# Optimization experiments

Measured on AMD Instinct MI355X. Metric: run time of the kernel, lower is better.

Reference implementation:

```python
import jax, jax.numpy as jnp
import numpy as np

V = 32000   # vocab
E = 512     # hidden_size (d_model)
NH = 8      # num_heads
DH = E // NH
NL = 2      # num_layers
FF = 2048   # TransformerDecoderLayer default dim_feedforward
MAXLEN = 24 # cfg.max_length -> gen_len (no target given)
S, B = 48, 8
TRANS = 14
INIT = TRANS - 2            # tgt = transform[1:-1]
LF = INIT + MAXLEN - 1      # final tgt length after the loop
EPS = 1e-5
NEG = -1e9


def pos_encoding(length, d):
    pos = np.arange(length, dtype=np.float32)[:, None]
    div = np.exp(-np.log(10000.0) * np.arange(0, d, 2, dtype=np.float32) / d)
    pe = np.zeros((length, d), dtype=np.float32)
    pe[:, 0::2] = np.sin(pos * div)
    pe[:, 1::2] = np.cos(pos * div)
    return jnp.asarray(pe)


def setup_inputs() -> dict:
    key = jax.random.key(0)
    ks = jax.random.split(key, 12)
    s = 0.02
    return {
        "enc_outputs": jax.random.normal(ks[0], (S, B, E), jnp.float32),
        "transform": jax.random.randint(ks[1], (TRANS, B), 0, V),
        "tf_ratio": 0,
        "emb_table": jax.random.normal(ks[2], (V, E), jnp.float32) * s,
        "sa_w": jax.random.normal(ks[3], (NL, 3 * E, E), jnp.float32) * s,
        "sa_b": jnp.zeros((NL, 3 * E), jnp.float32),
        "sa_ow": jax.random.normal(ks[4], (NL, E, E), jnp.float32) * s,
        "sa_ob": jnp.zeros((NL, E), jnp.float32),
        "ca_w": jax.random.normal(ks[5], (NL, 3 * E, E), jnp.float32) * s,
        "ca_b": jnp.zeros((NL, 3 * E), jnp.float32),
        "ca_ow": jax.random.normal(ks[6], (NL, E, E), jnp.float32) * s,
        "ca_ob": jnp.zeros((NL, E), jnp.float32),
        "ff1_w": jax.random.normal(ks[7], (NL, FF, E), jnp.float32) * s,
        "ff1_b": jnp.zeros((NL, FF), jnp.float32),
        "ff2_w": jax.random.normal(ks[8], (NL, E, FF), jnp.float32) * s,
        "ff2_b": jnp.zeros((NL, E), jnp.float32),
        "ln_g": jnp.ones((NL, 3, E), jnp.float32),
        "ln_b": jnp.zeros((NL, 3, E), jnp.float32),
        "out_w": jax.random.normal(ks[9], (V, E), jnp.float32) * s,
        "out_b": jnp.zeros((V,), jnp.float32),
    }


def _ln(x, g, b):
    m = jnp.mean(x, -1, keepdims=True)
    v = jnp.mean((x - m) ** 2, -1, keepdims=True)
    return (x - m) * jax.lax.rsqrt(v + EPS) * g + b


def _mha(q_in, kv_in, w, b, ow, ob, mask):
    # q_in [Lq,B,E], kv_in [Lk,B,E]; PyTorch packed in_proj [3E,E]
    wq, wk, wv = jnp.split(w, 3, 0)
    bq, bk, bv = jnp.split(b, 3, 0)
    proj = lambda x, wm, bm: (x @ wm.T + bm).reshape(x.shape[0], x.shape[1], NH, DH)
    q, k, v = proj(q_in, wq, bq), proj(kv_in, wk, bk), proj(kv_in, wv, bv)
    sc = jnp.einsum('qbhd,kbhd->bhqk', q, k) / np.sqrt(DH).astype(np.float32)
    if mask is not None:
        sc = sc + mask
    a = jax.nn.softmax(sc, -1)
    o = jnp.einsum('bhqk,kbhd->qbhd', a, v).reshape(q_in.shape[0], q_in.shape[1], E)
    return o @ ow.T + ob


def _decoder(x, mem, mask, p):
    # post-norm TransformerDecoderLayer: self-attn -> cross-attn -> relu FFN
    for l in range(NL):
        x = _ln(x + _mha(x, x, p['sa_w'][l], p['sa_b'][l], p['sa_ow'][l], p['sa_ob'][l], mask),
                p['ln_g'][l, 0], p['ln_b'][l, 0])
        x = _ln(x + _mha(x, mem, p['ca_w'][l], p['ca_b'][l], p['ca_ow'][l], p['ca_ob'][l], None),
                p['ln_g'][l, 1], p['ln_b'][l, 1])
        h = jax.nn.relu(x @ p['ff1_w'][l].T + p['ff1_b'][l]) @ p['ff2_w'][l].T + p['ff2_b'][l]
        x = _ln(x + h, p['ln_g'][l, 2], p['ln_b'][l, 2])
    return x


def reference(enc_outputs, transform, tf_ratio, emb_table, sa_w, sa_b, sa_ow, sa_ob,
              ca_w, ca_b, ca_ow, ca_ob, ff1_w, ff1_b, ff2_w, ff2_b, ln_g, ln_b,
              out_w, out_b):
    # tf_ratio == 0 -> no teacher forcing; gen_len = max_length (no target attr)
    p = dict(sa_w=sa_w, sa_b=sa_b, sa_ow=sa_ow, sa_ob=sa_ob, ca_w=ca_w, ca_b=ca_b,
             ca_ow=ca_ow, ca_ob=ca_ob, ff1_w=ff1_w, ff1_b=ff1_b, ff2_w=ff2_w,
             ff2_b=ff2_b, ln_g=ln_g, ln_b=ln_b)
    pe = pos_encoding(MAXLEN, E)
    # causal mask over the fixed-size buffer; padded (future) slots cannot
    # influence valid positions, so full-buffer passes == torch prefix passes.
    mask = jnp.where(jnp.tril(jnp.ones((LF, LF), bool)), 0.0, NEG)
    tgt0 = emb_table[transform[1:-1]] + pe[:INIT][:, None, :]   # [INIT,B,E]
    buf = jnp.zeros((LF, B, E), jnp.float32).at[:INIT].set(tgt0)

    def step(buf, i):
        h = _decoder(buf, enc_outputs, mask, p)
        pos = INIT - 1 + i                        # last valid position
        pred = jnp.argmax(h[pos] @ out_w.T + out_b, axis=-1)   # [B]
        # torch re-embeds the single predicted token -> PE position 0
        emb = emb_table[pred] + pe[0]
        return buf.at[pos + 1].set(emb), None

    buf, _ = jax.lax.scan(step, buf, jnp.arange(MAXLEN - 1))
    h = _decoder(buf, enc_outputs, mask, p)       # final loop iteration's pass
    return h @ out_w.T + out_b                    # dec_outputs [LF,B,V]
```

## Files before the change

### kernel.cpp

```cpp
#include <hip/hip_runtime.h>
#include <hip/hip_bf16.h>
#include <math.h>

#define V    32000
#define E    512
#define NH   8
#define DH   64
#define NL   2
#define FF   2048
#define MAXLEN 24
#define S    48
#define B    8
#define TRANS 14
#define INIT 12
#define LF   35

#define NB   256
#define NT   1024

typedef float f4 __attribute__((ext_vector_type(4)));

__device__ inline float wsum(float v) {
#pragma unroll
  for (int off = 32; off; off >>= 1) v += __shfl_xor(v, off);
  return v;
}
__device__ inline float wmax(float v) {
#pragma unroll
  for (int off = 32; off; off >>= 1) v = fmaxf(v, __shfl_xor(v, off));
  return v;
}

__device__ inline void stc(float* p, float v) {
  __hip_atomic_store(p, v, __ATOMIC_RELAXED, __HIP_MEMORY_SCOPE_AGENT);
}
__device__ inline void stc8(float* p, float x, float y) {
  union { unsigned long long u; float f[2]; } c; c.f[0] = x; c.f[1] = y;
  __hip_atomic_store((unsigned long long*)p, c.u, __ATOMIC_RELAXED, __HIP_MEMORY_SCOPE_AGENT);
}
__device__ inline int ldci(const int* p) {
  return __hip_atomic_load(p, __ATOMIC_RELAXED, __HIP_MEMORY_SCOPE_AGENT);
}
__device__ inline void stci(int* p, int v) {
  __hip_atomic_store(p, v, __ATOMIC_RELAXED, __HIP_MEMORY_SCOPE_AGENT);
}

#define CMB(v, idx, ov, oi) do { if ((ov) > (v) || ((ov) == (v) && (oi) < (idx))) { (v) = (ov); (idx) = (oi); } } while (0)


__global__ void embed_init_k(const int* __restrict__ transform, const float* __restrict__ emb,
                             float* __restrict__ xbuf) {
  int t = blockIdx.x;
  int pos = t >> 3, b = t & 7;
  int tok = transform[(1 + pos) * B + b];
  for (int d = threadIdx.x; d < E; d += blockDim.x) {
    double div = exp(-log(10000.0) * (double)(d & ~1) / (double)E);
    double ang = (double)pos * div;
    float pe = (d & 1) ? (float)cos(ang) : (float)sin(ang);
    xbuf[(size_t)t * E + d] = emb[(size_t)tok * E + d] + pe;
  }
}

template <int K>
__global__ __launch_bounds__(256) void gemm_k(
    const float* __restrict__ x, const float* __restrict__ W, const float* __restrict__ bias,
    int ntok, int nout, int route, int relu,
    float* __restrict__ out0, float* __restrict__ out1, float* __restrict__ out2) {
  constexpr int K4 = K / 4;
  constexpr int J  = K / 256;
  __shared__ float4 xt[8][K4];
  const int tid = threadIdx.x;
  const int lane = tid & 63;
  const int o = blockIdx.x * 4 + (tid >> 6);

  float4 wr[J];
  if (o < nout) {
    const float4* Wr = (const float4*)(W + (size_t)o * K);
#pragma unroll
    for (int j = 0; j < J; ++j) wr[j] = Wr[lane + 64 * j];
  }

  const int ng = ntok >> 3;
  for (int g = 0; g < ng; ++g) {
    if (g) __syncthreads();
    const float4* xg = (const float4*)(x + (size_t)g * 8 * K);
    float4* xf = &xt[0][0];
    for (int i = tid; i < 8 * K4; i += 256) xf[i] = xg[i];
    __syncthreads();
    if (o < nout) {
      float acc[8] = {0, 0, 0, 0, 0, 0, 0, 0};
#pragma unroll
      for (int j = 0; j < J; ++j) {
        float4 w = wr[j];
#pragma unroll
        for (int tt = 0; tt < 8; ++tt) {
          float4 xv = xt[tt][lane + 64 * j];
          acc[tt] += w.x * xv.x + w.y * xv.y + w.z * xv.z + w.w * xv.w;
        }
      }
#pragma unroll
      for (int tt = 0; tt < 8; ++tt) acc[tt] = wsum(acc[tt]);
      if (lane == 0) {
        float bo = bias[o];
#pragma unroll
        for (int tt = 0; tt < 8; ++tt) {
          float v = acc[tt] + bo;
          if (relu) v = fmaxf(v, 0.f);
          int t = g * 8 + tt;
          if (route == 0) {
            out0[(size_t)t * nout + o] = v;
          } else if (route == 1) {
            if (o < E) out0[(size_t)t * E + o] = v;
            else if (o < 2 * E) out1[(size_t)t * E + (o - E)] = v;
            else out2[(size_t)t * E + (o - 2 * E)] = v;
          } else {
            if (o < E) out0[(size_t)t * E + o] = v;
            else out1[(size_t)t * E + (o - E)] = v;
          }
        }
      }
    }
  }
}

__global__ __launch_bounds__(256) void attn_k(
    const float* __restrict__ q, const float* __restrict__ Kc, const float* __restrict__ Vc,
    float* __restrict__ outp, int p0, int nq, int nk_fixed, int causal) {
  const int tid = threadIdx.x;
  const int lane = tid & 63;
  const int u = blockIdx.x * 4 + (tid >> 6);
  if (u >= nq * 64) return;
  const int qi = u >> 6;
  const int r = u & 63;
  const int b = r >> 3, h = r & 7;
  const int nk = causal ? (p0 + qi + 1) : nk_fixed;

  const size_t qoff = (size_t)(qi * B + b) * E + h * DH + lane;
  const float qv = q[qoff];

  float myscore = -INFINITY;
  for (int k = 0; k < nk; ++k) {
    float prod = qv * Kc[(size_t)(k * B + b) * E + h * DH + lane];
    prod = wsum(prod);
    if (lane == k) myscore = prod * 0.125f;
  }
  float m = wmax(myscore);
  float p = (lane < nk) ? expf(myscore - m) : 0.f;
  float denom = wsum(p);
  float a = p / denom;

  float oacc = 0.f;
  for (int k = 0; k < nk; ++k) {
    float ak = __shfl(a, k);
    oacc = fmaf(ak, Vc[(size_t)(k * B + b) * E + h * DH + lane], oacc);
  }
  outp[qoff] = oacc;
}

__global__ __launch_bounds__(256) void add_ln_k(
    const float* __restrict__ xa, const float* __restrict__ xb,
    const float* __restrict__ g, const float* __restrict__ beta,
    float* __restrict__ outp, int ntok) {
  const int tid = threadIdx.x, lane = tid & 63;
  const int t = blockIdx.x * 4 + (tid >> 6);
  if (t >= ntok) return;
  float v[8];
  float s = 0.f;
#pragma unroll
  for (int j = 0; j < 8; ++j) {
    int d = lane + 64 * j;
    v[j] = xa[(size_t)t * E + d] + xb[(size_t)t * E + d];
    s += v[j];
  }
  s = wsum(s);
  float mean = s * (1.f / 512.f);
  float d2 = 0.f;
#pragma unroll
  for (int j = 0; j < 8; ++j) { float dd = v[j] - mean; d2 += dd * dd; }
  d2 = wsum(d2);
  float inv = 1.f / sqrtf(d2 * (1.f / 512.f) + 1e-5f);
#pragma unroll
  for (int j = 0; j < 8; ++j) {
    int d = lane + 64 * j;
    outp[(size_t)t * E + d] = (v[j] - mean) * inv * g[d] + beta[d];
  }
}

#define B_QKV 0
#define B_OW  6144
#define B_CQ  8192
#define B_COW 10240
#define B_FF1 12288
#define B_FF2 20480
#define SW_TOT 28672
#define SLOTS_PER_STEP 23
#define NSTAGE 17

__global__ __launch_bounds__(NT, 1) void decode_persist_k(
    const float* __restrict__ emb,
    const float* __restrict__ sa_w, const float* __restrict__ sa_b,
    const float* __restrict__ sa_ow, const float* __restrict__ sa_ob,
    const float* __restrict__ ca_w, const float* __restrict__ ca_b,
    const float* __restrict__ ca_ow, const float* __restrict__ ca_ob,
    const float* __restrict__ ff1_w, const float* __restrict__ ff1_b,
    const float* __restrict__ ff2_w, const float* __restrict__ ff2_b,
    const float* __restrict__ ln_g, const float* __restrict__ ln_b,
    const float* __restrict__ out_w, const float* __restrict__ out_b,
    float* __restrict__ kself, float* __restrict__ vself,
    const float* __restrict__ kcross, const float* __restrict__ vcross,
    float* __restrict__ arena, float* __restrict__ outp, int* __restrict__ bar) {
  __shared__ __align__(16) float s_w[SW_TOT];
  __shared__ __align__(16) float s_x[8 * E];
  __shared__ __align__(16) float s_raw[8 * E];
  __shared__ __align__(16) float s_q2[64];
  __shared__ __align__(16) float s_attw[64];
  __shared__ __align__(16) float s_part[4][64];
  __shared__ int   s_tok[8];
  __shared__ float s_pv[16][8];
  __shared__ int   s_pi[16][8];

  const int tid  = threadIdx.x;
  const int lane = tid & 63;
  const int wv   = tid >> 6;
  const int bid  = blockIdx.x;

  auto slot = [&](int st, int s) -> float* {
    return arena + ((size_t)st * SLOTS_PER_STEP + s) * 4096;
  };

  auto flg = [&](int s, int j) -> int* { return &bar[(s * 256 + j) * 16]; };

  auto set_flag = [&](int s, int tgt, bool producer) {
    __syncthreads();
    if (producer && tid == 0) stci(flg(s, bid), tgt);
  };
  auto wait_flags = [&](int s, int base, int count, int tgt) {
    if (wv == 0) {
      const int m = count - 1;
      for (;;) {
        bool ok = true;
        for (int f = lane; f < count; f += 64)
          ok &= (ldci(flg(s, base + ((f + bid) & m))) >= tgt);
        if (__all(ok)) break;
        __builtin_amdgcn_s_sleep(12);
      }
    }
    __syncthreads();
  };

  auto stage_raw = [&](const float* src) {
    const float4* s4 = (const float4*)src;
    float4* d4 = (float4*)s_raw;
    for (int k = tid; k < 1024; k += NT) d4[k] = s4[k];
    __syncthreads();
  };
  auto lnstage = [&](int lnidx) {
    if (wv < 8) {
      const float* gg = ln_g + (size_t)lnidx * E;
      const float* be = ln_b + (size_t)lnidx * E;
      float v[8]; float sum = 0.f;
#pragma unroll
      for (int j = 0; j < 8; ++j) {
        int d = lane + 64 * j;
        v[j] = s_x[wv * E + d] + s_raw[wv * E + d];
        sum += v[j];
      }
      sum = wsum(sum);
      float mean = sum * (1.f / 512.f);
      float d2 = 0.f;
#pragma unroll
      for (int j = 0; j < 8; ++j) { float dd = v[j] - mean; d2 += dd * dd; }
      d2 = wsum(d2);
      float inv = 1.f / sqrtf(d2 * (1.f / 512.f) + 1e-5f);
#pragma unroll
      for (int j = 0; j < 8; ++j) {
        int d = lane + 64 * j;
        s_x[wv * E + d] = (v[j] - mean) * inv * gg[d] + be[d];
      }
    }
    __syncthreads();
  };
  auto proj16 = [&](int wbase, const float* srcLDS, const float* biasp, float* dst) {
    int j = wv & 1, b = wv >> 1;
    int r = bid * 2 + j;
    const f4* wp = (const f4*)&s_w[wbase + j * 512];
    f4 w0 = wp[lane], w1 = wp[lane + 64];
    const f4* x4 = (const f4*)(srcLDS + b * E);
    f4 a = w0 * x4[lane] + w1 * x4[lane + 64];
    float acc = a.x + a.y + a.z + a.w;
    acc = wsum(acc);
    if (lane == 0) stc(&dst[b * E + r], acc + biasp[r]);
  };
  auto attn_stage = [&](const float* qsrc, const float* Kbase, const float* Vbase,
                        int nk, float* attdst) {
    const int b = bid >> 3, h = bid & 7;
    if (wv == 0) {
      s_q2[lane] = qsrc[b * E + h * DH + lane];
      float sc = -INFINITY;
      if (lane < nk) {
        const f4* Kr = (const f4*)(Kbase + ((size_t)lane * B + b) * E + h * DH);
        const f4* Qp = (const f4*)s_q2;
        float a0 = 0.f;
#pragma unroll
        for (int u = 0; u < 16; ++u) {
          f4 kv = Kr[u], qq = Qp[u];
          a0 += kv.x * qq.x + kv.y * qq.y + kv.z * qq.z + kv.w * qq.w;
        }
        sc = a0 * 0.125f;
      }
      float m = wmax(sc);
      float e = (lane < nk) ? expf(sc - m) : 0.f;
      float den = wsum(e);
      s_attw[lane] = e / den;
    }
    __syncthreads();
    if (wv < 4) {
      float o = 0.f;
      for (int k = wv; k < nk; k += 4)
        o = fmaf(s_attw[k], Vbase[((size_t)k * B + b) * E + h * DH + lane], o);
      s_part[wv][lane] = o;
    }
    __syncthreads();
    if (wv == 0)
      stc(&attdst[b * E + h * DH + lane],
          s_part[0][lane] + s_part[1][lane] + s_part[2][lane] + s_part[3][lane]);
  };

  {
    auto cprow = [&](const float* src, int dstf) {
      f4* d = (f4*)&s_w[dstf]; const f4* s = (const f4*)src;
      for (int k = tid; k < 128; k += NT) d[k] = s[k];
    };
    for (int l = 0; l < NL; ++l) {
      for (int j = 0; j < 6; ++j)
        cprow(sa_w + ((size_t)l * 1536 + bid * 6 + j) * E, B_QKV + (l * 6 + j) * 512);
      for (int j = 0; j < 2; ++j) {
        cprow(sa_ow + ((size_t)l * 512 + bid * 2 + j) * E, B_OW + (l * 2 + j) * 512);
        cprow(ca_w + ((size_t)l * 1536 + bid * 2 + j) * E, B_CQ + (l * 2 + j) * 512);
        cprow(ca_ow + ((size_t)l * 512 + bid * 2 + j) * E, B_COW + (l * 2 + j) * 512);
      }
      for (int j = 0; j < 8; ++j)
        cprow(ff1_w + ((size_t)l * FF + bid * 8 + j) * E, B_FF1 + (l * 8 + j) * 512);
    }
    const int lf2 = bid >> 7;
    for (int j = 0; j < 4; ++j) {
      f4* d = (f4*)&s_w[B_FF2 + j * 2048];
      const f4* s = (const f4*)(ff2_w + ((size_t)lf2 * 512 + (bid & 127) * 4 + j) * FF);
      for (int k = tid; k < 512; k += NT) d[k] = s[k];
    }
    __syncthreads();
  }

  for (int i = 0; i < MAXLEN - 1; ++i) {
    const int p = INIT + i;
    const int tgt = i + 1;
    float* amax_o = slot(i, 0);

    if (i > 0) wait_flags(16, 0, 256, i);
    {
      int bw = wv & 7;
      float v = -INFINITY; int ix = 0x7fffffff;
      if (i == 0) {
        const float2* row = (const float2*)(outp + ((size_t)(INIT - 1) * B + bw) * V);
        for (int jj = lane; jj < V / 2; jj += 64) {
          float2 t = row[jj];
          CMB(v, ix, t.x, 2 * jj);
          CMB(v, ix, t.y, 2 * jj + 1);
        }
      } else {
        const float2* ap = (const float2*)slot(i - 1, 0);
#pragma unroll
        for (int t = 0; t < 4; ++t) {
          int e = lane * 4 + t;
          float2 pr = ap[e * 8 + bw];
          CMB(v, ix, pr.x, (int)pr.y);
        }
      }
#pragma unroll
      for (int off = 1; off < 64; off <<= 1) {
        float ov = __shfl_xor(v, off); int oi = __shfl_xor(ix, off);
        CMB(v, ix, ov, oi);
      }
      if (lane == 0 && wv < 8) s_tok[bw] = ix;
      __syncthreads();
      int b = tid >> 7, d0 = (tid & 127) * 4;
      int tok = s_tok[b];
      float4 ev = *(const float4*)(emb + (size_t)tok * E + d0);
      s_x[b * E + d0]     = ev.x;
      s_x[b * E + d0 + 1] = ev.y + 1.0f;
      s_x[b * E + d0 + 2] = ev.z;
      s_x[b * E + d0 + 3] = ev.w + 1.0f;
      __syncthreads();
    }

    for (int l = 0; l < NL; ++l) {
      const int sb = l * 8;
      float* Lb    = slot(i, 1 + l * 11);
      float* q_s   = Lb;
      float* att_s = Lb + 4096;
      float* raw_s = Lb + 8192;
      float* q_c   = Lb + 12288;
      float* att_c = Lb + 16384;
      float* raw_c = Lb + 20480;
      float* hb    = Lb + 24576;
      float* yb    = Lb + 40960;

      if (wv < 12) {
        int j = wv >> 1, bg = (wv & 1) * 4;
        int r = bid * 6 + j, sec = r >> 9, off = r & 511;
        const f4* wp = (const f4*)&s_w[B_QKV + (l * 6 + j) * 512];
        f4 w0 = wp[lane], w1 = wp[lane + 64];
        float bias = sa_b[(size_t)l * 1536 + r];
        for (int b = bg; b < bg + 4; ++b) {
          const f4* x4 = (const f4*)&s_x[b * E];
          f4 a = w0 * x4[lane] + w1 * x4[lane + 64];
          float acc = a.x + a.y + a.z + a.w;
          acc = wsum(acc);
          if (lane == 0) {
            acc += bias;
            if (sec == 0) stc(&q_s[b * E + off], acc);
            else if (sec == 1) stc(&kself[((size_t)(l * LF + p) * B + b) * E + off], acc);
            else stc(&vself[((size_t)(l * LF + p) * B + b) * E + off], acc);
          }
        }
      }
      set_flag(sb + 0, tgt, true);
      wait_flags(sb + 0, 0, 256, tgt);
      if (bid < 64)
        attn_stage(q_s, kself + (size_t)l * LF * B * E, vself + (size_t)l * LF * B * E,
                   p + 1, att_s);
      set_flag(sb + 1, tgt, bid < 64);
      wait_flags(sb + 1, 0, 64, tgt);
      stage_raw(att_s);
      proj16(B_OW + l * 1024, s_raw, sa_ob + (size_t)l * E, raw_s);
      set_flag(sb + 2, tgt, true);
      wait_flags(sb + 2, 0, 256, tgt);
      stage_raw(raw_s);
      lnstage(l * 3 + 0);
      proj16(B_CQ + l * 1024, s_x, ca_b + (size_t)l * 3 * E, q_c);
      set_flag(sb + 3, tgt, true);
      wait_flags(sb + 3, 0, 256, tgt);
      if (bid < 64)
        attn_stage(q_c, kcross + (size_t)l * S * B * E, vcross + (size_t)l * S * B * E,
                   S, att_c);
      set_flag(sb + 4, tgt, bid < 64);
      wait_flags(sb + 4, 0, 64, tgt);
      stage_raw(att_c);
      proj16(B_COW + l * 1024, s_raw, ca_ob + (size_t)l * E, raw_c);
      set_flag(sb + 5, tgt, true);
      wait_flags(sb + 5, 0, 256, tgt);
      stage_raw(raw_c);
      lnstage(l * 3 + 1);
      {
        int j = wv >> 1, bg = (wv & 1) * 4;
        int r = bid * 8 + j;
        const f4* wp = (const f4*)&s_w[B_FF1 + (l * 8 + j) * 512];
        f4 w0 = wp[lane], w1 = wp[lane + 64];
        float bias = ff1_b[(size_t)l * FF + r];
        for (int b = bg; b < bg + 4; ++b) {
          const f4* x4 = (const f4*)&s_x[b * E];
          f4 a = w0 * x4[lane] + w1 * x4[lane + 64];
          float acc = a.x + a.y + a.z + a.w;
          acc = wsum(acc);
          if (lane == 0) stc(&hb[b * FF + r], fmaxf(acc + bias, 0.f));
        }
      }
      set_flag(sb + 6, tgt, true);
      wait_flags(sb + 6, 0, 256, tgt);
      if ((bid >> 7) == l) {
        int b = wv >> 1, j0 = (wv & 1) * 2;
        int r0 = (bid & 127) * 4;
        const f4* h4 = (const f4*)(hb + b * FF);
        f4 hv[8];
#pragma unroll
        for (int j = 0; j < 8; ++j) hv[j] = h4[j * 64 + lane];
#pragma unroll
        for (int jr = 0; jr < 2; ++jr) {
          int rl = j0 + jr;
          const f4* wp = (const f4*)&s_w[B_FF2 + rl * 2048];
          float acc = 0.f;
#pragma unroll
          for (int j = 0; j < 8; ++j) {
            f4 w = wp[j * 64 + lane];
            acc += w.x * hv[j].x + w.y * hv[j].y + w.z * hv[j].z + w.w * hv[j].w;
          }
          acc = wsum(acc);
          if (lane == 0)
            stc(&yb[b * E + r0 + rl], acc + ff2_b[(size_t)l * 512 + r0 + rl]);
        }
      }
      set_flag(sb + 7, tgt, (bid >> 7) == l);
      wait_flags(sb + 7, l * 128, 128, tgt);
      stage_raw(yb);
      lnstage(l * 3 + 2);
    }

    {
      const int grp = lane >> 3, sub = lane & 7;
      const int idx = wv * 8 + grp;
      const bool valid = idx < 125;
      const int r = bid * 125 + idx;
      float acc[8] = {0, 0, 0, 0, 0, 0, 0, 0};
      if (valid) {
        const f4* wrow = (const f4*)(out_w + (size_t)r * E);
#pragma unroll
        for (int half = 0; half < 2; ++half) {
          f4 w8[8];
#pragma unroll
          for (int j = 0; j < 8; ++j) w8[j] = wrow[(half * 8 + j) * 8 + sub];
#pragma unroll
          for (int b = 0; b < 8; ++b) {
            const f4* x4 = (const f4*)&s_x[b * E];
            float a = 0.f;
#pragma unroll
            for (int j = 0; j < 8; ++j) {
              f4 xx = x4[(half * 8 + j) * 8 + sub];
              a += w8[j].x * xx.x + w8[j].y * xx.y + w8[j].z * xx.z + w8[j].w * xx.w;
            }
            acc[b] += a;
          }
        }
#pragma unroll
        for (int b = 0; b < 8; ++b) {
          acc[b] += __shfl_xor(acc[b], 1);
          acc[b] += __shfl_xor(acc[b], 2);
          acc[b] += __shfl_xor(acc[b], 4);
        }
        if (sub == 0) {
          float bo = out_b[r];
#pragma unroll
          for (int b = 0; b < 8; ++b) {
            acc[b] += bo;
            outp[((size_t)p * B + b) * V + r] = acc[b];
          }
        }
      }
#pragma unroll
      for (int b = 0; b < 8; ++b) {
        float v = (valid && sub == 0) ? acc[b] : -INFINITY;
        int ix = (valid && sub == 0) ? r : 0x7fffffff;
#pragma unroll
        for (int off = 1; off < 64; off <<= 1) {
          float ov = __shfl_xor(v, off); int oi = __shfl_xor(ix, off);
          CMB(v, ix, ov, oi);
        }
        if (lane == 0) { s_pv[wv][b] = v; s_pi[wv][b] = ix; }
      }
      __syncthreads();
      if (wv == 0) {
        int b = lane & 7, w2 = lane >> 3;
        float v = s_pv[w2][b]; int ix = s_pi[w2][b];
        float v2 = s_pv[w2 + 8][b]; int ix2 = s_pi[w2 + 8][b];
        CMB(v, ix, v2, ix2);
#pragma unroll
        for (int off = 8; off < 64; off <<= 1) {
          float ov = __shfl_xor(v, off); int oi = __shfl_xor(ix, off);
          CMB(v, ix, ov, oi);
        }
        if (lane < 8) stc8(&amax_o[(size_t)(bid * 8 + lane) * 2], v, (float)ix);
      }
    }
    set_flag(16, tgt, true);
  }
}

extern "C" void kernel_launch(void* const* d_in, const int* in_sizes, int n_in,
                              void* d_out, int out_size, void* d_ws, size_t ws_size,
                              hipStream_t stream) {
  const float* enc       = (const float*)d_in[0];
  const int*   transform = (const int*)d_in[1];
  const float* emb       = (const float*)d_in[3];
  const float* sa_w  = (const float*)d_in[4];
  const float* sa_b  = (const float*)d_in[5];
  const float* sa_ow = (const float*)d_in[6];
  const float* sa_ob = (const float*)d_in[7];
  const float* ca_w  = (const float*)d_in[8];
  const float* ca_b  = (const float*)d_in[9];
  const float* ca_ow = (const float*)d_in[10];
  const float* ca_ob = (const float*)d_in[11];
  const float* ff1_w = (const float*)d_in[12];
  const float* ff1_b = (const float*)d_in[13];
  const float* ff2_w = (const float*)d_in[14];
  const float* ff2_b = (const float*)d_in[15];
  const float* ln_g  = (const float*)d_in[16];
  const float* ln_b  = (const float*)d_in[17];
  const float* out_w = (const float*)d_in[18];
  const float* out_b = (const float*)d_in[19];
  float* out = (float*)d_out;

  const size_t SELF_SZ  = (size_t)LF * B * E;
  const size_t CROSS_SZ = (size_t)S * B * E;
  const size_t ARENA_SZ = (size_t)(MAXLEN - 1) * SLOTS_PER_STEP * 4096;
  const size_t FLAG_SZ  = (size_t)NSTAGE * 256 * 16;
  float* ws     = (float*)d_ws;
  float* xbuf   = ws;
  float* kself  = xbuf + (size_t)INIT * B * E;
  float* vself  = kself + NL * SELF_SZ;
  float* kcross = vself + NL * SELF_SZ;
  float* vcross = kcross + NL * CROSS_SZ;
  float* arena  = vcross + NL * CROSS_SZ;
  int*   bar    = (int*)(arena + ARENA_SZ);
  float* act1   = (float*)(bar + FLAG_SZ);
  float* act2   = act1 + 96 * E;
  float* act3   = act2 + 96 * E;
  float* ffb    = act3 + 96 * E;

  hipMemsetAsync(bar, 0, FLAG_SZ * 4, stream);

  embed_init_k<<<INIT * B, 128, 0, stream>>>(transform, emb, xbuf);

  for (int l = 0; l < NL; ++l) {
    gemm_k<E><<<(2 * E) / 4, 256, 0, stream>>>(
        enc, ca_w + ((size_t)l * 3 * E + E) * E, ca_b + (size_t)l * 3 * E + E,
        S * B, 2 * E, 2, 0, kcross + l * CROSS_SZ, vcross + l * CROSS_SZ, nullptr);
  }

  {
    const int p0 = 0, nq = INIT, ntok = nq * B;
    const float* xin = xbuf;
    for (int l = 0; l < NL; ++l) {
      const float* x = (l == 0) ? xin : act1;
      gemm_k<E><<<(3 * E) / 4, 256, 0, stream>>>(
          x, sa_w + (size_t)l * 3 * E * E, sa_b + (size_t)l * 3 * E, ntok, 3 * E, 1, 0,
          act2, kself + l * SELF_SZ, vself + l * SELF_SZ);
      attn_k<<<nq * 16, 256, 0, stream>>>(act2, kself + l * SELF_SZ, vself + l * SELF_SZ,
                                          act3, p0, nq, 0, 1);
      gemm_k<E><<<E / 4, 256, 0, stream>>>(
          act3, sa_ow + (size_t)l * E * E, sa_ob + (size_t)l * E, ntok, E, 0, 0, act2, nullptr, nullptr);
      add_ln_k<<<(ntok + 3) / 4, 256, 0, stream>>>(
          x, act2, ln_g + (size_t)l * 3 * E, ln_b + (size_t)l * 3 * E, act1, ntok);
      gemm_k<E><<<E / 4, 256, 0, stream>>>(
          act1, ca_w + (size_t)l * 3 * E * E, ca_b + (size_t)l * 3 * E, ntok, E, 0, 0, act2, nullptr, nullptr);
      attn_k<<<nq * 16, 256, 0, stream>>>(act2, kcross + l * CROSS_SZ, vcross + l * CROSS_SZ,
                                          act3, p0, nq, S, 0);
      gemm_k<E><<<E / 4, 256, 0, stream>>>(
          act3, ca_ow + (size_t)l * E * E, ca_ob + (size_t)l * E, ntok, E, 0, 0, act2, nullptr, nullptr);
      add_ln_k<<<(ntok + 3) / 4, 256, 0, stream>>>(
          act1, act2, ln_g + (size_t)l * 3 * E + E, ln_b + (size_t)l * 3 * E + E, act1, ntok);
      gemm_k<E><<<FF / 4, 256, 0, stream>>>(
          act1, ff1_w + (size_t)l * FF * E, ff1_b + (size_t)l * FF, ntok, FF, 0, 1, ffb, nullptr, nullptr);
      gemm_k<FF><<<E / 4, 256, 0, stream>>>(
          ffb, ff2_w + (size_t)l * E * FF, ff2_b + (size_t)l * E, ntok, E, 0, 0, act2, nullptr, nullptr);
      add_ln_k<<<(ntok + 3) / 4, 256, 0, stream>>>(
          act1, act2, ln_g + (size_t)l * 3 * E + 2 * E, ln_b + (size_t)l * 3 * E + 2 * E, act1, ntok);
    }
    gemm_k<E><<<V / 4, 256, 0, stream>>>(
        act1, out_w, out_b, ntok, V, 0, 0, out, nullptr, nullptr);
  }

  decode_persist_k<<<NB, NT, 0, stream>>>(
      emb, sa_w, sa_b, sa_ow, sa_ob, ca_w, ca_b, ca_ow, ca_ob,
      ff1_w, ff1_b, ff2_w, ff2_b, ln_g, ln_b, out_w, out_b,
      kself, vself, kcross, vcross, arena, out, bar);
}
```

Before: 5.071 ms.

## Fold prefill and cross-KV projection into the persistent decode kernel

Removes the separate prefill launches (cross K/V GEMMs, per-layer QKV, attention, projections, layernorms, FFN, vocab GEMM) and performs them inside the persistent kernel as extra flag-synchronised stages. The prefill argmax is also fused so the first decode step reads precomputed per-block maxima instead of rescanning the logits row. This targets the launch overhead and the serial gaps of about two dozen small kernels. In exchange the prefill runs under grid-wide flag barriers with per-block GEMV tiling, which may use the hardware less efficiently than the old dedicated GEMM kernels and adds more barrier stages.

```diff
diff --git a/kernel.cpp b/kernel.cpp
--- a/kernel.cpp
+++ b/kernel.cpp
@@ -47,7 +47,6 @@
 
 #define CMB(v, idx, ov, oi) do { if ((ov) > (v) || ((ov) == (v) && (oi) < (idx))) { (v) = (ov); (idx) = (oi); } } while (0)
 
-
 __global__ void embed_init_k(const int* __restrict__ transform, const float* __restrict__ emb,
                              float* __restrict__ xbuf) {
   int t = blockIdx.x;
@@ -61,131 +60,6 @@
   }
 }
 
-template <int K>
-__global__ __launch_bounds__(256) void gemm_k(
-    const float* __restrict__ x, const float* __restrict__ W, const float* __restrict__ bias,
-    int ntok, int nout, int route, int relu,
-    float* __restrict__ out0, float* __restrict__ out1, float* __restrict__ out2) {
-  constexpr int K4 = K / 4;
-  constexpr int J  = K / 256;
-  __shared__ float4 xt[8][K4];
-  const int tid = threadIdx.x;
-  const int lane = tid & 63;
-  const int o = blockIdx.x * 4 + (tid >> 6);
-
-  float4 wr[J];
-  if (o < nout) {
-    const float4* Wr = (const float4*)(W + (size_t)o * K);
-#pragma unroll
-    for (int j = 0; j < J; ++j) wr[j] = Wr[lane + 64 * j];
-  }
-
-  const int ng = ntok >> 3;
-  for (int g = 0; g < ng; ++g) {
-    if (g) __syncthreads();
-    const float4* xg = (const float4*)(x + (size_t)g * 8 * K);
-    float4* xf = &xt[0][0];
-    for (int i = tid; i < 8 * K4; i += 256) xf[i] = xg[i];
-    __syncthreads();
-    if (o < nout) {
-      float acc[8] = {0, 0, 0, 0, 0, 0, 0, 0};
-#pragma unroll
-      for (int j = 0; j < J; ++j) {
-        float4 w = wr[j];
-#pragma unroll
-        for (int tt = 0; tt < 8; ++tt) {
-          float4 xv = xt[tt][lane + 64 * j];
-          acc[tt] += w.x * xv.x + w.y * xv.y + w.z * xv.z + w.w * xv.w;
-        }
-      }
-#pragma unroll
-      for (int tt = 0; tt < 8; ++tt) acc[tt] = wsum(acc[tt]);
-      if (lane == 0) {
-        float bo = bias[o];
-#pragma unroll
-        for (int tt = 0; tt < 8; ++tt) {
-          float v = acc[tt] + bo;
-          if (relu) v = fmaxf(v, 0.f);
-          int t = g * 8 + tt;
-          if (route == 0) {
-            out0[(size_t)t * nout + o] = v;
-          } else if (route == 1) {
-            if (o < E) out0[(size_t)t * E + o] = v;
-            else if (o < 2 * E) out1[(size_t)t * E + (o - E)] = v;
-            else out2[(size_t)t * E + (o - 2 * E)] = v;
-          } else {
-            if (o < E) out0[(size_t)t * E + o] = v;
-            else out1[(size_t)t * E + (o - E)] = v;
-          }
-        }
-      }
-    }
-  }
-}
-
-__global__ __launch_bounds__(256) void attn_k(
-    const float* __restrict__ q, const float* __restrict__ Kc, const float* __restrict__ Vc,
-    float* __restrict__ outp, int p0, int nq, int nk_fixed, int causal) {
-  const int tid = threadIdx.x;
-  const int lane = tid & 63;
-  const int u = blockIdx.x * 4 + (tid >> 6);
-  if (u >= nq * 64) return;
-  const int qi = u >> 6;
-  const int r = u & 63;
-  const int b = r >> 3, h = r & 7;
-  const int nk = causal ? (p0 + qi + 1) : nk_fixed;
-
-  const size_t qoff = (size_t)(qi * B + b) * E + h * DH + lane;
-  const float qv = q[qoff];
-
-  float myscore = -INFINITY;
-  for (int k = 0; k < nk; ++k) {
-    float prod = qv * Kc[(size_t)(k * B + b) * E + h * DH + lane];
-    prod = wsum(prod);
-    if (lane == k) myscore = prod * 0.125f;
-  }
-  float m = wmax(myscore);
-  float p = (lane < nk) ? expf(myscore - m) : 0.f;
-  float denom = wsum(p);
-  float a = p / denom;
-
-  float oacc = 0.f;
-  for (int k = 0; k < nk; ++k) {
-    float ak = __shfl(a, k);
-    oacc = fmaf(ak, Vc[(size_t)(k * B + b) * E + h * DH + lane], oacc);
-  }
-  outp[qoff] = oacc;
-}
-
-__global__ __launch_bounds__(256) void add_ln_k(
-    const float* __restrict__ xa, const float* __restrict__ xb,
-    const float* __restrict__ g, const float* __restrict__ beta,
-    float* __restrict__ outp, int ntok) {
-  const int tid = threadIdx.x, lane = tid & 63;
-  const int t = blockIdx.x * 4 + (tid >> 6);
-  if (t >= ntok) return;
-  float v[8];
-  float s = 0.f;
-#pragma unroll
-  for (int j = 0; j < 8; ++j) {
-    int d = lane + 64 * j;
-    v[j] = xa[(size_t)t * E + d] + xb[(size_t)t * E + d];
-    s += v[j];
-  }
-  s = wsum(s);
-  float mean = s * (1.f / 512.f);
-  float d2 = 0.f;
-#pragma unroll
-  for (int j = 0; j < 8; ++j) { float dd = v[j] - mean; d2 += dd * dd; }
-  d2 = wsum(d2);
-  float inv = 1.f / sqrtf(d2 * (1.f / 512.f) + 1e-5f);
-#pragma unroll
-  for (int j = 0; j < 8; ++j) {
-    int d = lane + 64 * j;
-    outp[(size_t)t * E + d] = (v[j] - mean) * inv * g[d] + beta[d];
-  }
-}
-
 #define B_QKV 0
 #define B_OW  6144
 #define B_CQ  8192
@@ -194,10 +68,23 @@
 #define B_FF2 20480
 #define SW_TOT 28672
 #define SLOTS_PER_STEP 23
-#define NSTAGE 17
+#define NSTAGE 41
+
+#define PRE_L   688128
+#define PQ_OFF  0
+#define PATTS   49152
+#define PRAWS   98304
+#define PX1     147456
+#define PQC     196608
+#define PATTC   245760
+#define PRAWC   294912
+#define PX2     344064
+#define PY      393216
+#define PX3     442368
+#define PHB     491520
 
 __global__ __launch_bounds__(NT, 1) void decode_persist_k(
-    const float* __restrict__ emb,
+    const float* __restrict__ enc, const float* __restrict__ emb,
     const float* __restrict__ sa_w, const float* __restrict__ sa_b,
     const float* __restrict__ sa_ow, const float* __restrict__ sa_ob,
     const float* __restrict__ ca_w, const float* __restrict__ ca_b,
@@ -206,8 +93,9 @@
     const float* __restrict__ ff2_w, const float* __restrict__ ff2_b,
     const float* __restrict__ ln_g, const float* __restrict__ ln_b,
     const float* __restrict__ out_w, const float* __restrict__ out_b,
+    const float* __restrict__ xpre, float* __restrict__ pre, float* __restrict__ amax_pre,
     float* __restrict__ kself, float* __restrict__ vself,
-    const float* __restrict__ kcross, const float* __restrict__ vcross,
+    float* __restrict__ kcross, float* __restrict__ vcross,
     float* __restrict__ arena, float* __restrict__ outp, int* __restrict__ bar) {
   __shared__ __align__(16) float s_w[SW_TOT];
   __shared__ __align__(16) float s_x[8 * E];
@@ -223,13 +111,12 @@
   const int lane = tid & 63;
   const int wv   = tid >> 6;
   const int bid  = blockIdx.x;
+  const size_t CROSS_SZ = (size_t)S * B * E;
 
   auto slot = [&](int st, int s) -> float* {
     return arena + ((size_t)st * SLOTS_PER_STEP + s) * 4096;
   };
-
   auto flg = [&](int s, int j) -> int* { return &bar[(s * 256 + j) * 16]; };
-
   auto set_flag = [&](int s, int tgt, bool producer) {
     __syncthreads();
     if (producer && tid == 0) stci(flg(s, bid), tgt);
@@ -247,84 +134,292 @@
     }
     __syncthreads();
   };
-
   auto stage_raw = [&](const float* src) {
     const float4* s4 = (const float4*)src;
     float4* d4 = (float4*)s_raw;
     for (int k = tid; k < 1024; k += NT) d4[k] = s4[k];
     __syncthreads();
   };
-  auto lnstage = [&](int lnidx) {
-    if (wv < 8) {
-      const float* gg = ln_g + (size_t)lnidx * E;
-      const float* be = ln_b + (size_t)lnidx * E;
-      float v[8]; float sum = 0.f;
-#pragma unroll
-      for (int j = 0; j < 8; ++j) {
-        int d = lane + 64 * j;
-        v[j] = s_x[wv * E + d] + s_raw[wv * E + d];
-        sum += v[j];
-      }
-      sum = wsum(sum);
-      float mean = sum * (1.f / 512.f);
-      float d2 = 0.f;
-#pragma unroll
-      for (int j = 0; j < 8; ++j) { float dd = v[j] - mean; d2 += dd * dd; }
-      d2 = wsum(d2);
-      float inv = 1.f / sqrtf(d2 * (1.f / 512.f) + 1e-5f);
-#pragma unroll
-      for (int j = 0; j < 8; ++j) {
-        int d = lane + 64 * j;
-        s_x[wv * E + d] = (v[j] - mean) * inv * gg[d] + be[d];
-      }
-    }
-    __syncthreads();
-  };
-  auto proj16 = [&](int wbase, const float* srcLDS, const float* biasp, float* dst) {
-    int j = wv & 1, b = wv >> 1;
+  auto ln_vec = [&](const float* xa, const float* xb, int lnidx, float* dst) {
+    const float* gg = ln_g + (size_t)lnidx * E;
+    const float* be = ln_b + (size_t)lnidx * E;
+    float v[8]; float sum = 0.f;
+#pragma unroll
+    for (int j = 0; j < 8; ++j) {
+      int d = lane + 64 * j;
+      v[j] = xa[d] + xb[d];
+      sum += v[j];
+    }
+    sum = wsum(sum);
+    float mean = sum * (1.f / 512.f);
+    float d2 = 0.f;
+#pragma unroll
+    for (int j = 0; j < 8; ++j) { float dd = v[j] - mean; d2 += dd * dd; }
+    d2 = wsum(d2);
+    float inv = 1.f / sqrtf(d2 * (1.f / 512.f) + 1e-5f);
+#pragma unroll
+    for (int j = 0; j < 8; ++j) {
+      int d = lane + 64 * j;
+      stc(&dst[d], (v[j] - mean) * inv * gg[d] + be[d]);
+    }
+  };
+  auto pproj = [&](const float* Wb, const float* biasp, const float* src, float* dst) {
+    int j = wv >> 3, tt = wv & 7;
     int r = bid * 2 + j;
-    const f4* wp = (const f4*)&s_w[wbase + j * 512];
+    const f4* wp = (const f4*)(Wb + (size_t)r * E);
     f4 w0 = wp[lane], w1 = wp[lane + 64];
-    const f4* x4 = (const f4*)(srcLDS + b * E);
-    f4 a = w0 * x4[lane] + w1 * x4[lane + 64];
-    float acc = a.x + a.y + a.z + a.w;
-    acc = wsum(acc);
-    if (lane == 0) stc(&dst[b * E + r], acc + biasp[r]);
-  };
-  auto attn_stage = [&](const float* qsrc, const float* Kbase, const float* Vbase,
-                        int nk, float* attdst) {
-    const int b = bid >> 3, h = bid & 7;
-    if (wv == 0) {
-      s_q2[lane] = qsrc[b * E + h * DH + lane];
-      float sc = -INFINITY;
-      if (lane < nk) {
-        const f4* Kr = (const f4*)(Kbase + ((size_t)lane * B + b) * E + h * DH);
-        const f4* Qp = (const f4*)s_q2;
-        float a0 = 0.f;
-#pragma unroll
-        for (int u = 0; u < 16; ++u) {
-          f4 kv = Kr[u], qq = Qp[u];
-          a0 += kv.x * qq.x + kv.y * qq.y + kv.z * qq.z + kv.w * qq.w;
-        }
-        sc = a0 * 0.125f;
-      }
-      float m = wmax(sc);
-      float e = (lane < nk) ? expf(sc - m) : 0.f;
-      float den = wsum(e);
-      s_attw[lane] = e / den;
-    }
-    __syncthreads();
-    if (wv < 4) {
-      float o = 0.f;
-      for (int k = wv; k < nk; k += 4)
-        o = fmaf(s_attw[k], Vbase[((size_t)k * B + b) * E + h * DH + lane], o);
-      s_part[wv][lane] = o;
-    }
-    __syncthreads();
-    if (wv == 0)
-      stc(&attdst[b * E + h * DH + lane],
-          s_part[0][lane] + s_part[1][lane] + s_part[2][lane] + s_part[3][lane]);
-  };
+    float bias = biasp[r];
+    for (int g = 0; g < 12; ++g) {
+      stage_raw(src + (size_t)g * 8 * E);
+      const f4* x4 = (const f4*)&s_raw[tt * E];
+      f4 a = w0 * x4[lane] + w1 * x4[lane + 64];
+      float acc = a.x + a.y + a.z + a.w;
+      acc = wsum(acc);
+      if (lane == 0) stc(&dst[(size_t)(g * 8 + tt) * E + r], acc + bias);
+      __syncthreads();
+    }
+  };
+
+  {
+    for (int l = 0; l < NL; ++l) {
+      const int rr = (bid >> 2) * 16 + wv;
+      const int sec = rr >> 9, off = rr & 511;
+      const f4* wp = (const f4*)(ca_w + ((size_t)l * 1536 + 512 + rr) * E);
+      f4 w0 = wp[lane], w1 = wp[lane + 64];
+      float bias = ca_b[(size_t)l * 1536 + 512 + rr];
+      float* dst = (sec == 0 ? kcross : vcross) + (size_t)l * CROSS_SZ;
+      for (int g = 0; g < 12; ++g) {
+        int t0 = (bid & 3) * 96 + g * 8;
+        stage_raw(enc + (size_t)t0 * E);
+        for (int tt = 0; tt < 8; ++tt) {
+          const f4* x4 = (const f4*)&s_raw[tt * E];
+          f4 a = w0 * x4[lane] + w1 * x4[lane + 64];
+          float acc = a.x + a.y + a.z + a.w;
+          acc = wsum(acc);
+          if (lane == 0) stc(&dst[(size_t)(t0 + tt) * E + off], acc + bias);
+        }
+        __syncthreads();
+      }
+    }
+    set_flag(39, 1, true);
+
+    for (int l = 0; l < NL; ++l) {
+      const int PB = 17 + l * 11;
+      float* PL = pre + (size_t)l * PRE_L;
+      float* q_l = PL + PQ_OFF;  float* attS_l = PL + PATTS; float* rawS_l = PL + PRAWS;
+      float* x1_l = PL + PX1;    float* qc_l = PL + PQC;     float* attC_l = PL + PATTC;
+      float* rawC_l = PL + PRAWC; float* x2_l = PL + PX2;    float* y_l = PL + PY;
+      float* x3_l = PL + PX3;    float* hb_l = PL + PHB;
+      const float* xsrc = (l == 0) ? xpre : (pre + PX3);
+
+      if (l == 1) wait_flags(17 + 10, 0, 128, 1);
+      {
+        int j = wv >> 1, bg = (wv & 1) * 4;
+        int r = bid * 6 + j, sec = r >> 9, off = r & 511;
+        f4 w0, w1; float bias = 0.f;
+        if (wv < 12) {
+          const f4* wp = (const f4*)(sa_w + ((size_t)l * 1536 + r) * E);
+          w0 = wp[lane]; w1 = wp[lane + 64];
+          bias = sa_b[(size_t)l * 1536 + r];
+        }
+        for (int g = 0; g < 12; ++g) {
+          stage_raw(xsrc + (size_t)g * 8 * E);
+          if (wv < 12) {
+            for (int tt = bg; tt < bg + 4; ++tt) {
+              const f4* x4 = (const f4*)&s_raw[tt * E];
+              f4 a = w0 * x4[lane] + w1 * x4[lane + 64];
+              float acc = a.x + a.y + a.z + a.w;
+              acc = wsum(acc);
+              if (lane == 0) {
+                int t = g * 8 + tt; acc += bias;
+                if (sec == 0) stc(&q_l[(size_t)t * E + off], acc);
+                else if (sec == 1) stc(&kself[((size_t)l * LF * B + t) * E + off], acc);
+                else stc(&vself[((size_t)l * LF * B + t) * E + off], acc);
+              }
+            }
+          }
+          __syncthreads();
+        }
+      }
+      set_flag(PB + 0, 1, true);
+      wait_flags(PB + 0, 0, 256, 1);
+      if (bid < 48) {
+        int u = bid * 16 + wv, qi = u >> 6, rr = u & 63, b = rr >> 3, h = rr & 7;
+        int nk = qi + 1;
+        float qv = q_l[(size_t)(qi * 8 + b) * E + h * DH + lane];
+        float sc = -INFINITY;
+        for (int k = 0; k < nk; ++k) {
+          float pr = wsum(qv * kself[((size_t)l * LF * B + k * 8 + b) * E + h * DH + lane]);
+          if (lane == k) sc = pr * 0.125f;
+        }
+        float m = wmax(sc);
+        float e = (lane < nk) ? expf(sc - m) : 0.f;
+        float den = wsum(e);
+        float aa = e / den, o = 0.f;
+        for (int k = 0; k < nk; ++k) {
+          float ak = __shfl(aa, k);
+          o = fmaf(ak, vself[((size_t)l * LF * B + k * 8 + b) * E + h * DH + lane], o);
+        }
+        stc(&attS_l[(size_t)(qi * 8 + b) * E + h * DH + lane], o);
+      }
+      set_flag(PB + 1, 1, bid < 64);
+      wait_flags(PB + 1, 0, 64, 1);
+      pproj(sa_ow + (size_t)l * 512 * E, sa_ob + (size_t)l * 512, attS_l, rawS_l);
+      set_flag(PB + 2, 1, true);
+      wait_flags(PB + 2, 0, 256, 1);
+      if (bid < 96 && wv == 0)
+        ln_vec(xsrc + (size_t)bid * E, rawS_l + (size_t)bid * E, l * 3 + 0, x1_l + (size_t)bid * E);
+      set_flag(PB + 3, 1, bid < 128);
+      wait_flags(PB + 3, 0, 128, 1);
+      pproj(ca_w + (size_t)l * 1536 * E, ca_b + (size_t)l * 1536, x1_l, qc_l);
+      set_flag(PB + 4, 1, true);
+      wait_flags(PB + 4, 0, 256, 1);
+      wait_flags(39, 0, 256, 1);
+      if (bid < 48) {
+        int u = bid * 16 + wv, qi = u >> 6, rr = u & 63, b = rr >> 3, h = rr & 7;
+        const float* Kc = kcross + (size_t)l * CROSS_SZ;
+        const float* Vc = vcross + (size_t)l * CROSS_SZ;
+        float qv = qc_l[(size_t)(qi * 8 + b) * E + h * DH + lane];
+        float sc = -INFINITY;
+        for (int k = 0; k < S; ++k) {
+          float pr = wsum(qv * Kc[(size_t)(k * 8 + b) * E + h * DH + lane]);
+          if (lane == k) sc = pr * 0.125f;
+        }
+        float m = wmax(sc);
+        float e = (lane < S) ? expf(sc - m) : 0.f;
+        float den = wsum(e);
+        float aa = e / den, o = 0.f;
+        for (int k = 0; k < S; ++k) {
+          float ak = __shfl(aa, k);
+          o = fmaf(ak, Vc[(size_t)(k * 8 + b) * E + h * DH + lane], o);
+        }
+        stc(&attC_l[(size_t)(qi * 8 + b) * E + h * DH + lane], o);
+      }
+      set_flag(PB + 5, 1, bid < 64);
+      wait_flags(PB + 5, 0, 64, 1);
+      pproj(ca_ow + (size_t)l * 512 * E, ca_ob + (size_t)l * 512, attC_l, rawC_l);
+      set_flag(PB + 6, 1, true);
+      wait_flags(PB + 6, 0, 256, 1);
+      if (bid < 96 && wv == 0)
+        ln_vec(x1_l + (size_t)bid * E, rawC_l + (size_t)bid * E, l * 3 + 1, x2_l + (size_t)bid * E);
+      set_flag(PB + 7, 1, bid < 128);
+      wait_flags(PB + 7, 0, 128, 1);
+      {
+        int j = wv >> 1, bg = (wv & 1) * 4;
+        int r = bid * 8 + j;
+        const f4* wp = (const f4*)(ff1_w + ((size_t)l * FF + r) * E);
+        f4 w0 = wp[lane], w1 = wp[lane + 64];
+        float bias = ff1_b[(size_t)l * FF + r];
+        for (int g = 0; g < 12; ++g) {
+          stage_raw(x2_l + (size_t)g * 8 * E);
+          for (int tt = bg; tt < bg + 4; ++tt) {
+            const f4* x4 = (const f4*)&s_raw[tt * E];
+            f4 a = w0 * x4[lane] + w1 * x4[lane + 64];
+            float acc = a.x + a.y + a.z + a.w;
+            acc = wsum(acc);
+            if (lane == 0)
+              stc(&hb_l[(size_t)(g * 8 + tt) * FF + r], fmaxf(acc + bias, 0.f));
+          }
+          __syncthreads();
+        }
+      }
+      set_flag(PB + 8, 1, true);
+      wait_flags(PB + 8, 0, 256, 1);
+      if ((bid >> 7) == l) {
+        int r0 = (bid & 127) * 4;
+        for (int u = wv; u < 384; u += 16) {
+          int t = u >> 2, rl = u & 3;
+          const f4* h4 = (const f4*)(hb_l + (size_t)t * FF);
+          const f4* wp = (const f4*)(ff2_w + ((size_t)l * 512 + r0 + rl) * FF);
+          float acc = 0.f;
+#pragma unroll
+          for (int j = 0; j < 8; ++j) {
+            f4 hv = h4[j * 64 + lane];
+            f4 w = wp[j * 64 + lane];
+            acc += w.x * hv.x + w.y * hv.y + w.z * hv.z + w.w * hv.w;
+          }
+          acc = wsum(acc);
+          if (lane == 0)
+            stc(&y_l[(size_t)t * E + r0 + rl], acc + ff2_b[(size_t)l * 512 + r0 + rl]);
+        }
+      }
+      set_flag(PB + 9, 1, (bid >> 7) == l);
+      wait_flags(PB + 9, l * 128, 128, 1);
+      if (bid < 96 && wv == 0)
+        ln_vec(x2_l + (size_t)bid * E, y_l + (size_t)bid * E, l * 3 + 2, x3_l + (size_t)bid * E);
+      set_flag(PB + 10, 1, bid < 128);
+    }
+
+    wait_flags(17 + 11 + 10, 0, 128, 1);
+    {
+      float* s_acc = s_w;
+      const float* x3f = pre + PRE_L + PX3;
+      const int grp = lane >> 3, sub = lane & 7;
+      const int idx = wv * 8 + grp;
+      const bool valid = idx < 125;
+      const int r = bid * 125 + idx;
+      for (int k = tid; k < 128 * 96; k += NT) s_acc[k] = 0.f;
+      __syncthreads();
+      for (int half = 0; half < 2; ++half) {
+        f4 w8[8];
+        if (valid) {
+          const f4* wrow = (const f4*)(out_w + (size_t)r * E);
+#pragma unroll
+          for (int j = 0; j < 8; ++j) w8[j] = wrow[(half * 8 + j) * 8 + sub];
+        }
+        for (int g = 0; g < 12; ++g) {
+          stage_raw(x3f + (size_t)g * 8 * E);
+          if (valid) {
+            for (int b = 0; b < 8; ++b) {
+              const f4* x4 = (const f4*)&s_raw[b * E];
+              float a = 0.f;
+#pragma unroll
+              for (int j = 0; j < 8; ++j) {
+                f4 xx = x4[(half * 8 + j) * 8 + sub];
+                a += w8[j].x * xx.x + w8[j].y * xx.y + w8[j].z * xx.z + w8[j].w * xx.w;
+              }
+              a += __shfl_xor(a, 1);
+              a += __shfl_xor(a, 2);
+              a += __shfl_xor(a, 4);
+              if (sub == 0) s_acc[idx * 96 + g * 8 + b] += a;
+            }
+          }
+          __syncthreads();
+        }
+      }
+      if (valid) {
+        float bo = out_b[r];
+        for (int k = sub; k < 96; k += 8)
+          outp[(size_t)k * V + r] = s_acc[idx * 96 + k] + bo;
+      }
+      __syncthreads();
+      for (int b = 0; b < 8; ++b) {
+        float v = (valid && sub == 0) ? s_acc[idx * 96 + 88 + b] + out_b[r] : -INFINITY;
+        int ix = (valid && sub == 0) ? r : 0x7fffffff;
+#pragma unroll
+        for (int off = 1; off < 64; off <<= 1) {
+          float ov = __shfl_xor(v, off); int oi = __shfl_xor(ix, off);
+          CMB(v, ix, ov, oi);
+        }
+        if (lane == 0) { s_pv[wv][b] = v; s_pi[wv][b] = ix; }
+      }
+      __syncthreads();
+      if (wv == 0) {
+        int b = lane & 7, w2 = lane >> 3;
+        float v = s_pv[w2][b]; int ix = s_pi[w2][b];
+        float v2 = s_pv[w2 + 8][b]; int ix2 = s_pi[w2 + 8][b];
+        CMB(v, ix, v2, ix2);
+#pragma unroll
+        for (int off = 8; off < 64; off <<= 1) {
+          float ov = __shfl_xor(v, off); int oi = __shfl_xor(ix, off);
+          CMB(v, ix, ov, oi);
+        }
+        if (lane < 8) stc8(&amax_pre[(size_t)(bid * 8 + lane) * 2], v, (float)ix);
+      }
+      __syncthreads();
+    }
+    set_flag(40, 1, true);
+  }
 
   {
     auto cprow = [&](const float* src, int dstf) {
@@ -351,30 +446,94 @@
     __syncthreads();
   }
 
+  auto lnstage = [&](int lnidx) {
+    if (wv < 8) {
+      const float* gg = ln_g + (size_t)lnidx * E;
+      const float* be = ln_b + (size_t)lnidx * E;
+      float v[8]; float sum = 0.f;
+#pragma unroll
+      for (int j = 0; j < 8; ++j) {
+        int d = lane + 64 * j;
+        v[j] = s_x[wv * E + d] + s_raw[wv * E + d];
+        sum += v[j];
+      }
+      sum = wsum(sum);
+      float mean = sum * (1.f / 512.f);
+      float d2 = 0.f;
+#pragma unroll
+      for (int j = 0; j < 8; ++j) { float dd = v[j] - mean; d2 += dd * dd; }
+      d2 = wsum(d2);
+      float inv = 1.f / sqrtf(d2 * (1.f / 512.f) + 1e-5f);
+#pragma unroll
+      for (int j = 0; j < 8; ++j) {
+        int d = lane + 64 * j;
+        s_x[wv * E + d] = (v[j] - mean) * inv * gg[d] + be[d];
+      }
+    }
+    __syncthreads();
+  };
+  auto proj16 = [&](int wbase, const float* srcLDS, const float* biasp, float* dst) {
+    int j = wv & 1, b = wv >> 1;
+    int r = bid * 2 + j;
+    const f4* wp = (const f4*)&s_w[wbase + j * 512];
+    f4 w0 = wp[lane], w1 = wp[lane + 64];
+    const f4* x4 = (const f4*)(srcLDS + b * E);
+    f4 a = w0 * x4[lane] + w1 * x4[lane + 64];
+    float acc = a.x + a.y + a.z + a.w;
+    acc = wsum(acc);
+    if (lane == 0) stc(&dst[b * E + r], acc + biasp[r]);
+  };
+  auto attn_stage = [&](const float* qsrc, const float* Kbase, const float* Vbase,
+                        int nk, float* attdst) {
+    const int b = bid >> 3, h = bid & 7;
+    if (wv == 0) {
+      s_q2[lane] = qsrc[b * E + h * DH + lane];
+      float sc = -INFINITY;
+      if (lane < nk) {
+        const f4* Kr = (const f4*)(Kbase + ((size_t)lane * B + b) * E + h * DH);
+        const f4* Qp = (const f4*)s_q2;
+        float a0 = 0.f;
+#pragma unroll
+        for (int u = 0; u < 16; ++u) {
+          f4 kv = Kr[u], qq = Qp[u];
+          a0 += kv.x * qq.x + kv.y * qq.y + kv.z * qq.z + kv.w * qq.w;
+        }
+        sc = a0 * 0.125f;
+      }
+      float m = wmax(sc);
+      float e = (lane < nk) ? expf(sc - m) : 0.f;
+      float den = wsum(e);
+      s_attw[lane] = e / den;
+    }
+    __syncthreads();
+    if (wv < 4) {
+      float o = 0.f;
+      for (int k = wv; k < nk; k += 4)
+        o = fmaf(s_attw[k], Vbase[((size_t)k * B + b) * E + h * DH + lane], o);
+      s_part[wv][lane] = o;
+    }
+    __syncthreads();
+    if (wv == 0)
+      stc(&attdst[b * E + h * DH + lane],
+          s_part[0][lane] + s_part[1][lane] + s_part[2][lane] + s_part[3][lane]);
+  };
+
   for (int i = 0; i < MAXLEN - 1; ++i) {
     const int p = INIT + i;
     const int tgt = i + 1;
     float* amax_o = slot(i, 0);
 
-    if (i > 0) wait_flags(16, 0, 256, i);
+    if (i == 0) wait_flags(40, 0, 256, 1);
+    else        wait_flags(16, 0, 256, i);
     {
       int bw = wv & 7;
       float v = -INFINITY; int ix = 0x7fffffff;
-      if (i == 0) {
-        const float2* row = (const float2*)(outp + ((size_t)(INIT - 1) * B + bw) * V);
-        for (int jj = lane; jj < V / 2; jj += 64) {
-          float2 t = row[jj];
-          CMB(v, ix, t.x, 2 * jj);
-          CMB(v, ix, t.y, 2 * jj + 1);
-        }
-      } else {
-        const float2* ap = (const float2*)slot(i - 1, 0);
-#pragma unroll
-        for (int t = 0; t < 4; ++t) {
-          int e = lane * 4 + t;
-          float2 pr = ap[e * 8 + bw];
-          CMB(v, ix, pr.x, (int)pr.y);
-        }
+      const float2* ap = (i == 0) ? (const float2*)amax_pre : (const float2*)slot(i - 1, 0);
+#pragma unroll
+      for (int t = 0; t < 4; ++t) {
+        int e = lane * 4 + t;
+        float2 pr = ap[e * 8 + bw];
+        CMB(v, ix, pr.x, (int)pr.y);
       }
 #pragma unroll
       for (int off = 1; off < 64; off <<= 1) {
@@ -441,7 +600,7 @@
       set_flag(sb + 3, tgt, true);
       wait_flags(sb + 3, 0, 256, tgt);
       if (bid < 64)
-        attn_stage(q_c, kcross + (size_t)l * S * B * E, vcross + (size_t)l * S * B * E,
+        attn_stage(q_c, kcross + (size_t)l * CROSS_SZ, vcross + (size_t)l * CROSS_SZ,
                    S, att_c);
       set_flag(sb + 4, tgt, bid < 64);
       wait_flags(sb + 4, 0, 64, tgt);
@@ -593,63 +752,22 @@
   const size_t ARENA_SZ = (size_t)(MAXLEN - 1) * SLOTS_PER_STEP * 4096;
   const size_t FLAG_SZ  = (size_t)NSTAGE * 256 * 16;
   float* ws     = (float*)d_ws;
-  float* xbuf   = ws;
-  float* kself  = xbuf + (size_t)INIT * B * E;
+  float* xpre   = ws;
+  float* kself  = xpre + 96 * E;
   float* vself  = kself + NL * SELF_SZ;
   float* kcross = vself + NL * SELF_SZ;
   float* vcross = kcross + NL * CROSS_SZ;
   float* arena  = vcross + NL * CROSS_SZ;
-  int*   bar    = (int*)(arena + ARENA_SZ);
-  float* act1   = (float*)(bar + FLAG_SZ);
-  float* act2   = act1 + 96 * E;
-  float* act3   = act2 + 96 * E;
-  float* ffb    = act3 + 96 * E;
+  float* pre    = arena + ARENA_SZ;
+  float* amaxp  = pre + (size_t)NL * PRE_L;
+  int*   bar    = (int*)(amaxp + 4096);
 
   hipMemsetAsync(bar, 0, FLAG_SZ * 4, stream);
 
-  embed_init_k<<<INIT * B, 128, 0, stream>>>(transform, emb, xbuf);
-
-  for (int l = 0; l < NL; ++l) {
-    gemm_k<E><<<(2 * E) / 4, 256, 0, stream>>>(
-        enc, ca_w + ((size_t)l * 3 * E + E) * E, ca_b + (size_t)l * 3 * E + E,
-        S * B, 2 * E, 2, 0, kcross + l * CROSS_SZ, vcross + l * CROSS_SZ, nullptr);
-  }
-
-  {
-    const int p0 = 0, nq = INIT, ntok = nq * B;
-    const float* xin = xbuf;
-    for (int l = 0; l < NL; ++l) {
-      const float* x = (l == 0) ? xin : act1;
-      gemm_k<E><<<(3 * E) / 4, 256, 0, stream>>>(
-          x, sa_w + (size_t)l * 3 * E * E, sa_b + (size_t)l * 3 * E, ntok, 3 * E, 1, 0,
-          act2, kself + l * SELF_SZ, vself + l * SELF_SZ);
-      attn_k<<<nq * 16, 256, 0, stream>>>(act2, kself + l * SELF_SZ, vself + l * SELF_SZ,
-                                          act3, p0, nq, 0, 1);
-      gemm_k<E><<<E / 4, 256, 0, stream>>>(
-          act3, sa_ow + (size_t)l * E * E, sa_ob + (size_t)l * E, ntok, E, 0, 0, act2, nullptr, nullptr);
-      add_ln_k<<<(ntok + 3) / 4, 256, 0, stream>>>(
-          x, act2, ln_g + (size_t)l * 3 * E, ln_b + (size_t)l * 3 * E, act1, ntok);
-      gemm_k<E><<<E / 4, 256, 0, stream>>>(
-          act1, ca_w + (size_t)l * 3 * E * E, ca_b + (size_t)l * 3 * E, ntok, E, 0, 0, act2, nullptr, nullptr);
-      attn_k<<<nq * 16, 256, 0, stream>>>(act2, kcross + l * CROSS_SZ, vcross + l * CROSS_SZ,
-                                          act3, p0, nq, S, 0);
-      gemm_k<E><<<E / 4, 256, 0, stream>>>(
-          act3, ca_ow + (size_t)l * E * E, ca_ob + (size_t)l * E, ntok, E, 0, 0, act2, nullptr, nullptr);
-      add_ln_k<<<(ntok + 3) / 4, 256, 0, stream>>>(
-          act1, act2, ln_g + (size_t)l * 3 * E + E, ln_b + (size_t)l * 3 * E + E, act1, ntok);
-      gemm_k<E><<<FF / 4, 256, 0, stream>>>(
-          act1, ff1_w + (size_t)l * FF * E, ff1_b + (size_t)l * FF, ntok, FF, 0, 1, ffb, nullptr, nullptr);
-      gemm_k<FF><<<E / 4, 256, 0, stream>>>(
-          ffb, ff2_w + (size_t)l * E * FF, ff2_b + (size_t)l * E, ntok, E, 0, 0, act2, nullptr, nullptr);
-      add_ln_k<<<(ntok + 3) / 4, 256, 0, stream>>>(
-          act1, act2, ln_g + (size_t)l * 3 * E + 2 * E, ln_b + (size_t)l * 3 * E + 2 * E, act1, ntok);
-    }
-    gemm_k<E><<<V / 4, 256, 0, stream>>>(
-        act1, out_w, out_b, ntok, V, 0, 0, out, nullptr, nullptr);
-  }
+  embed_init_k<<<96, 128, 0, stream>>>(transform, emb, xpre);
 
   decode_persist_k<<<NB, NT, 0, stream>>>(
-      emb, sa_w, sa_b, sa_ow, sa_ob, ca_w, ca_b, ca_ow, ca_ob,
+      enc, emb, sa_w, sa_b, sa_ow, sa_ob, ca_w, ca_b, ca_ow, ca_ob,
       ff1_w, ff1_b, ff2_w, ff2_b, ln_g, ln_b, out_w, out_b,
-      kself, vself, kcross, vcross, arena, out, bar);
-}
+      xpre, pre, amaxp, kself, vself, kcross, vcross, arena, out, bar);
+}
```

Result: faster. 4.664 ms (median of 2 runs) (-8.0%).
